# Performance work log

Hardware: AMD Instinct MI355X
Metric: run time of the kernel (lower is better)

The kernel has to match this reference:

```python
import math
import jax, jax.numpy as jnp
import numpy as np

E = 8          # num_experts
H = 1024       # hidden_dim
F = 2048       # ffn_dim
TOP_K = 2
CAP_FACTOR = 1.25
B, S = 2, 2048


def setup_inputs() -> dict:
    key = jax.random.key(0)
    ks = jax.random.split(key, 7)
    xavier_gu = math.sqrt(2.0 / (H + F))
    return {
        "x": jax.random.normal(ks[0], (B, S, H), dtype=jnp.float32),
        "router_weight": 0.01 * jax.random.normal(ks[1], (H, E), dtype=jnp.float32),
        "w_gate": xavier_gu * jax.random.normal(ks[2], (E, H, F), dtype=jnp.float32),
        "w_up": xavier_gu * jax.random.normal(ks[3], (E, H, F), dtype=jnp.float32),
        "w_down": xavier_gu * jax.random.normal(ks[4], (E, F, H), dtype=jnp.float32),
        "ln_gamma": jnp.ones((H,), dtype=jnp.float32),
        "ln_beta": jnp.zeros((H,), dtype=jnp.float32),
    }


def _layernorm(x, g, b, eps=1e-5):
    mu = x.mean(-1, keepdims=True)
    var = ((x - mu) ** 2).mean(-1, keepdims=True)
    return (x - mu) / jnp.sqrt(var + eps) * g + b


def reference(x, router_weight, w_gate, w_up, w_down, ln_gamma, ln_beta):
    Bd, Sd, Hd = x.shape
    T = Bd * Sd
    cap = int(math.ceil(CAP_FACTOR * T / E))  # static capacity per expert

    residual = x
    tokens = _layernorm(x, ln_gamma, ln_beta).reshape(T, Hd)

    # ---- router: softmax + top-k + renormalize ----
    logits = tokens @ router_weight                      # (T, E) fp32
    probs = jax.nn.softmax(logits, axis=-1)
    wts, idx = jax.lax.top_k(probs, TOP_K)               # (T, K)
    wts = wts / wts.sum(-1, keepdims=True)

    # ---- dispatch: first-come-first-served up to capacity per expert ----
    mask_all = (idx[None, :, :] == jnp.arange(E)[:, None, None]).any(-1)  # (E, T)
    # stable argsort puts routed token indices (in order) first
    sel = jnp.argsort(jnp.where(mask_all, 0, 1), axis=1, stable=True)[:, :cap]  # (E, cap)
    valid = jnp.take_along_axis(mask_all, sel, axis=1)   # (E, cap)
    xin = tokens[sel] * valid[..., None]                 # (E, cap, H); zeros for empty slots

    # ---- grouped SwiGLU expert GEMMs ----
    gate = jax.nn.silu(jnp.einsum('ech,ehf->ecf', xin, w_gate))
    up = jnp.einsum('ech,ehf->ecf', xin, w_up)
    expert_outputs = jnp.einsum('ecf,efh->ech', gate * up, w_down)  # (E, cap, H)

    # ---- scatter-gather combine (slot = min(t, cap-1), per reference impl) ----
    slot = jnp.minimum(jnp.arange(T), cap - 1)           # (T,)
    gathered = expert_outputs[idx, slot[:, None]]        # (T, K, H)
    out = (wts[..., None] * gathered).sum(axis=1)        # (T, H)

    return out.reshape(Bd, Sd, Hd) + residual
```

## Files before the change

### kernel.cpp

```cpp
#include <hip/hip_runtime.h>
#include <hip/hip_bf16.h>

#define NE 8
#define NH 1024
#define NF 2048
#define NT 4096
#define CAP 640

typedef __bf16 bf16x8 __attribute__((ext_vector_type(8)));
typedef float f32x4 __attribute__((ext_vector_type(4)));

__device__ __forceinline__ ushort f2bf(float f) {
    union { float f; unsigned u; } v; v.f = f;
    unsigned r = (v.u + 0x7FFFu + ((v.u >> 16) & 1u)) >> 16;
    return (ushort)r;
}

__device__ __forceinline__ void glds16(const ushort* g, ushort* l) {
    __builtin_amdgcn_global_load_lds((const __attribute__((address_space(1))) void*)g,
                                     (__attribute__((address_space(3))) void*)l,
                                     16, 0, 0);
}

__global__ __launch_bounds__(256) void k_transpose(
    const float* __restrict__ in, ushort* __restrict__ out, int R, int C)
{
    int e = blockIdx.z;
    int c0 = blockIdx.x * 64, r0 = blockIdx.y * 64;
    in  += (size_t)e * R * C;
    out += (size_t)e * R * C;

    __shared__ __align__(16) ushort lds[64 * 72];
    int t = threadIdx.x;
    int rl = t >> 4;
    int cl = (t & 15) * 4;

    #pragma unroll
    for (int i = 0; i < 4; ++i) {
        int r = i * 16 + rl;
        float4 v = *(const float4*)(in + (size_t)(r0 + r) * C + c0 + cl);
        lds[(cl + 0) * 72 + r] = f2bf(v.x);
        lds[(cl + 1) * 72 + r] = f2bf(v.y);
        lds[(cl + 2) * 72 + r] = f2bf(v.z);
        lds[(cl + 3) * 72 + r] = f2bf(v.w);
    }
    __syncthreads();

    int c = t >> 2, rq = (t & 3) * 16;
    uint4 a = *(const uint4*)&lds[c * 72 + rq];
    uint4 b = *(const uint4*)&lds[c * 72 + rq + 8];
    *(uint4*)(out + (size_t)(c0 + c) * R + r0 + rq)     = a;
    *(uint4*)(out + (size_t)(c0 + c) * R + r0 + rq + 8) = b;
}

__global__ __launch_bounds__(256) void k_ln_router(
    const float* __restrict__ x, const float* __restrict__ rw,
    const float* __restrict__ gamma, const float* __restrict__ beta,
    ushort* __restrict__ tok_bf, int* __restrict__ idx, float* __restrict__ wts)
{
    int t = blockIdx.x, tid = threadIdx.x;
    int lane = tid & 63, wid = tid >> 6;
    const float* xp = x + (size_t)t * NH;

    float4 v = *(const float4*)(xp + tid * 4);
    float xs[4] = {v.x, v.y, v.z, v.w};
    float s = xs[0] + xs[1] + xs[2] + xs[3];
    float q = xs[0]*xs[0] + xs[1]*xs[1] + xs[2]*xs[2] + xs[3]*xs[3];

    __shared__ float rs[4], rq[4], rl[4][8];
    #pragma unroll
    for (int o = 32; o; o >>= 1) { s += __shfl_xor(s, o); q += __shfl_xor(q, o); }
    if (lane == 0) { rs[wid] = s; rq[wid] = q; }
    __syncthreads();
    float S = rs[0] + rs[1] + rs[2] + rs[3];
    float Q = rq[0] + rq[1] + rq[2] + rq[3];
    float mean = S * (1.0f / NH);
    float var  = Q * (1.0f / NH) - mean * mean;
    float rstd = 1.0f / sqrtf(var + 1e-5f);

    float le[8] = {0,0,0,0,0,0,0,0};
    ushort tb[4];
    #pragma unroll
    for (int j = 0; j < 4; ++j) {
        int h = tid * 4 + j;
        float nh = (xs[j] - mean) * rstd * gamma[h] + beta[h];
        tb[j] = f2bf(nh);
        float4 r0 = *(const float4*)(rw + h * 8);
        float4 r1 = *(const float4*)(rw + h * 8 + 4);
        le[0] += nh * r0.x; le[1] += nh * r0.y; le[2] += nh * r0.z; le[3] += nh * r0.w;
        le[4] += nh * r1.x; le[5] += nh * r1.y; le[6] += nh * r1.z; le[7] += nh * r1.w;
    }
    union { ushort s2[4]; uint2 u2; } pk;
    pk.s2[0]=tb[0]; pk.s2[1]=tb[1]; pk.s2[2]=tb[2]; pk.s2[3]=tb[3];
    *(uint2*)(tok_bf + (size_t)t * NH + tid * 4) = pk.u2;

    #pragma unroll
    for (int o = 32; o; o >>= 1)
        #pragma unroll
        for (int e = 0; e < 8; ++e) le[e] += __shfl_xor(le[e], o);
    if (lane == 0)
        #pragma unroll
        for (int e = 0; e < 8; ++e) rl[wid][e] = le[e];
    __syncthreads();

    if (tid == 0) {
        float l[8];
        #pragma unroll
        for (int e = 0; e < 8; ++e) l[e] = rl[0][e] + rl[1][e] + rl[2][e] + rl[3][e];
        float mx = l[0];
        #pragma unroll
        for (int e = 1; e < 8; ++e) mx = fmaxf(mx, l[e]);
        float p[8], den = 0.f;
        #pragma unroll
        for (int e = 0; e < 8; ++e) { p[e] = expf(l[e] - mx); den += p[e]; }
        float rden = 1.0f / den;
        #pragma unroll
        for (int e = 0; e < 8; ++e) p[e] *= rden;
        int i0 = 0; float b0 = p[0];
        #pragma unroll
        for (int e = 1; e < 8; ++e) if (p[e] > b0) { b0 = p[e]; i0 = e; }
        int i1 = (i0 == 0) ? 1 : 0; float b1 = p[i1];
        #pragma unroll
        for (int e = 0; e < 8; ++e) if (e != i0 && p[e] > b1) { b1 = p[e]; i1 = e; }
        float sw = 1.0f / (b0 + b1);
        idx[2*t] = i0; idx[2*t+1] = i1;
        wts[2*t] = b0 * sw; wts[2*t+1] = b1 * sw;
    }
}

__global__ __launch_bounds__(1024) void k_build_sel(
    const int* __restrict__ idx, int* __restrict__ sel)
{
    int e = blockIdx.x, tid = threadIdx.x;
    int lane = tid & 63, wid = tid >> 6;
    __shared__ int wsum[16], wpre[16], sbase;
    if (tid < CAP) sel[e * CAP + tid] = -1;
    if (tid == 0) sbase = 0;
    __syncthreads();

    for (int ch = 0; ch < NT / 1024; ++ch) {
        int t = ch * 1024 + tid;
        int m = (idx[2*t] == e || idx[2*t+1] == e) ? 1 : 0;
        int v = m;
        #pragma unroll
        for (int d = 1; d < 64; d <<= 1) {
            int u = __shfl_up(v, d);
            if (lane >= d) v += u;
        }
        if (lane == 63) wsum[wid] = v;
        __syncthreads();
        if (tid < 16) {
            int ws = wsum[tid], wv = ws;
            #pragma unroll
            for (int d = 1; d < 16; d <<= 1) {
                int u = __shfl_up(wv, d);
                if (tid >= d) wv += u;
            }
            wpre[tid] = wv - ws;
        }
        __syncthreads();
        int base0 = sbase;
        int slot = base0 + wpre[wid] + v - m;
        if (m && slot < CAP) sel[e * CAP + slot] = t;
        __syncthreads();
        if (tid == 0) sbase = base0 + wpre[15] + wsum[15];
        __syncthreads();
    }
}

__global__ __launch_bounds__(256) void k_gather(
    const int* __restrict__ sel, const ushort* __restrict__ tok,
    ushort* __restrict__ xin)
{
    int sIdx = blockIdx.x;
    int tokid = sel[sIdx];
    uint2 v = make_uint2(0u, 0u);
    if (tokid >= 0)
        v = *(const uint2*)(tok + (size_t)tokid * NH + threadIdx.x * 4);
    *(uint2*)(xin + (size_t)sIdx * NH + threadIdx.x * 4) = v;
}

__global__ __launch_bounds__(256) void k_gemm1(
    const ushort* __restrict__ xin, const ushort* __restrict__ wgT,
    const ushort* __restrict__ wuT, ushort* __restrict__ hb)
{
    int e = blockIdx.z, mb = blockIdx.y, nb = blockIdx.x;
    const ushort* A  = xin + (size_t)e * CAP * NH + (size_t)mb * 128 * NH;
    const ushort* Bg = wgT + (size_t)e * NF * NH + (size_t)nb * 128 * NH;
    const ushort* Bu = wuT + (size_t)e * NF * NH + (size_t)nb * 128 * NH;
    ushort* out = hb + (size_t)e * CAP * NF + (size_t)mb * 128 * NF + nb * 128;

    __shared__ __align__(16) ushort Al[128 * 32];
    __shared__ __align__(16) ushort Bgl[128 * 32];
    __shared__ __align__(16) ushort Bul[128 * 32];

    int tid = threadIdx.x, lane = tid & 63, wid = tid >> 6;
    int wm = wid >> 1, wn = wid & 1;
    int lr = lane & 15, lq = lane >> 4;
    int ldrow = lane >> 2;
    int lcol  = (lane & 3) * 8;

    f32x4 accg[4][4] = {}; f32x4 accu[4][4] = {};

    for (int k0 = 0; k0 < NH; k0 += 32) {
        #pragma unroll
        for (int i = 0; i < 2; ++i) {
            int row = i * 64 + wid * 16 + ldrow;
            int lb  = i * 2048 + wid * 512;
            glds16(A  + (size_t)row * NH + k0 + lcol, Al  + lb);
            glds16(Bg + (size_t)row * NH + k0 + lcol, Bgl + lb);
            glds16(Bu + (size_t)row * NH + k0 + lcol, Bul + lb);
        }
        __syncthreads();

        bf16x8 af[4], bgf[4], buf_[4];
        #pragma unroll
        for (int m = 0; m < 4; ++m)
            af[m] = *(const bf16x8*)&Al[(wm * 64 + m * 16 + lr) * 32 + lq * 8];
        #pragma unroll
        for (int n = 0; n < 4; ++n) {
            bgf[n]  = *(const bf16x8*)&Bgl[(wn * 64 + n * 16 + lr) * 32 + lq * 8];
            buf_[n] = *(const bf16x8*)&Bul[(wn * 64 + n * 16 + lr) * 32 + lq * 8];
        }
        #pragma unroll
        for (int m = 0; m < 4; ++m)
            #pragma unroll
            for (int n = 0; n < 4; ++n) {
                accg[m][n] = __builtin_amdgcn_mfma_f32_16x16x32_bf16(af[m], bgf[n],  accg[m][n], 0, 0, 0);
                accu[m][n] = __builtin_amdgcn_mfma_f32_16x16x32_bf16(af[m], buf_[n], accu[m][n], 0, 0, 0);
            }
        __syncthreads();
    }

    #pragma unroll
    for (int m = 0; m < 4; ++m)
        #pragma unroll
        for (int n = 0; n < 4; ++n)
            #pragma unroll
            for (int r = 0; r < 4; ++r) {
                int row = wm * 64 + m * 16 + lq * 4 + r;
                int col = wn * 64 + n * 16 + lr;
                float g = accg[m][n][r], u = accu[m][n][r];
                float sg = g / (1.0f + expf(-g));
                out[(size_t)row * NF + col] = f2bf(sg * u);
            }
}

__global__ __launch_bounds__(256) void k_gemm2(
    const ushort* __restrict__ hb, const ushort* __restrict__ wdT,
    float* __restrict__ eo)
{
    int e = blockIdx.z, mb = blockIdx.y, nb = blockIdx.x;
    const ushort* A = hb  + (size_t)e * CAP * NF + (size_t)mb * 128 * NF;
    const ushort* B = wdT + (size_t)e * NH * NF + (size_t)nb * 64 * NF;
    float* out = eo + (size_t)e * CAP * NH + (size_t)mb * 128 * NH + nb * 64;

    __shared__ __align__(16) ushort Al[128 * 32];
    __shared__ __align__(16) ushort Bl[64 * 32];

    int tid = threadIdx.x, lane = tid & 63, wid = tid >> 6;
    int wm = wid >> 1, wn = wid & 1;
    int lr = lane & 15, lq = lane >> 4;
    int ldrow = lane >> 2;
    int lcol  = (lane & 3) * 8;

    f32x4 acc[4][2] = {};

    for (int k0 = 0; k0 < NF; k0 += 32) {
        #pragma unroll
        for (int i = 0; i < 2; ++i) {
            int row = i * 64 + wid * 16 + ldrow;
            glds16(A + (size_t)row * NF + k0 + lcol, Al + i * 2048 + wid * 512);
        }
        glds16(B + (size_t)(wid * 16 + ldrow) * NF + k0 + lcol, Bl + wid * 512);
        __syncthreads();

        bf16x8 af[4], bf_[2];
        #pragma unroll
        for (int m = 0; m < 4; ++m)
            af[m] = *(const bf16x8*)&Al[(wm * 64 + m * 16 + lr) * 32 + lq * 8];
        #pragma unroll
        for (int n = 0; n < 2; ++n)
            bf_[n] = *(const bf16x8*)&Bl[(wn * 32 + n * 16 + lr) * 32 + lq * 8];
        #pragma unroll
        for (int m = 0; m < 4; ++m)
            #pragma unroll
            for (int n = 0; n < 2; ++n)
                acc[m][n] = __builtin_amdgcn_mfma_f32_16x16x32_bf16(af[m], bf_[n], acc[m][n], 0, 0, 0);
        __syncthreads();
    }

    #pragma unroll
    for (int m = 0; m < 4; ++m)
        #pragma unroll
        for (int n = 0; n < 2; ++n)
            #pragma unroll
            for (int r = 0; r < 4; ++r) {
                int row = wm * 64 + m * 16 + lq * 4 + r;
                int col = wn * 32 + n * 16 + lr;
                out[(size_t)row * NH + col] = acc[m][n][r];
            }
}

__global__ __launch_bounds__(256) void k_final(
    const float* __restrict__ x, const float* __restrict__ eo,
    const int* __restrict__ idx, const float* __restrict__ wts,
    float* __restrict__ out)
{
    int t = blockIdx.x;
    int c = (t < CAP - 1) ? t : (CAP - 1);
    int e0 = idx[2*t], e1 = idx[2*t+1];
    float w0 = wts[2*t], w1 = wts[2*t+1];
    int h = threadIdx.x * 4;
    float4 xv = *(const float4*)(x + (size_t)t * NH + h);
    float4 a = *(const float4*)(eo + ((size_t)e0 * CAP + c) * NH + h);
    float4 b = *(const float4*)(eo + ((size_t)e1 * CAP + c) * NH + h);
    float4 o;
    o.x = xv.x + w0 * a.x + w1 * b.x;
    o.y = xv.y + w0 * a.y + w1 * b.y;
    o.z = xv.z + w0 * a.z + w1 * b.z;
    o.w = xv.w + w0 * a.w + w1 * b.w;
    *(float4*)(out + (size_t)t * NH + h) = o;
}

extern "C" void kernel_launch(void* const* d_in, const int* in_sizes, int n_in,
                              void* d_out, int out_size, void* d_ws, size_t ws_size,
                              hipStream_t stream)
{
    const float* x     = (const float*)d_in[0];
    const float* rw    = (const float*)d_in[1];
    const float* wg    = (const float*)d_in[2];
    const float* wu    = (const float*)d_in[3];
    const float* wd    = (const float*)d_in[4];
    const float* gamma = (const float*)d_in[5];
    const float* beta  = (const float*)d_in[6];
    float* out = (float*)d_out;

    char* ws = (char*)d_ws;
    ushort* tok_bf = (ushort*)(ws);
    ushort* xin    = (ushort*)(ws +   8388608);
    ushort* hb     = (ushort*)(ws +  18874368);
    float*  eo     = (float*) (ws +  39845888);
    ushort* wgT    = (ushort*)(ws +  60817408);
    ushort* wuT    = (ushort*)(ws +  94371840);
    ushort* wdT    = (ushort*)(ws + 127926272);
    int*    idx    = (int*)   (ws + 161480704);
    float*  wts    = (float*) (ws + 161513472);
    int*    sel    = (int*)   (ws + 161546240);

    k_transpose<<<dim3(NF / 64, NH / 64, NE), 256, 0, stream>>>(wg, wgT, NH, NF);
    k_transpose<<<dim3(NF / 64, NH / 64, NE), 256, 0, stream>>>(wu, wuT, NH, NF);
    k_transpose<<<dim3(NH / 64, NF / 64, NE), 256, 0, stream>>>(wd, wdT, NF, NH);

    k_ln_router<<<NT, 256, 0, stream>>>(x, rw, gamma, beta, tok_bf, idx, wts);
    k_build_sel<<<NE, 1024, 0, stream>>>(idx, sel);
    k_gather<<<NE * CAP, 256, 0, stream>>>(sel, tok_bf, xin);
    k_gemm1<<<dim3(NF / 128, CAP / 128, NE), 256, 0, stream>>>(xin, wgT, wuT, hb);
    k_gemm2<<<dim3(NH / 64, CAP / 128, NE), 256, 0, stream>>>(hb, wdT, eo);
    k_final<<<NT, 256, 0, stream>>>(x, eo, idx, wts, out);
}
```

Baseline: 421.3 us.

## Rewrite expert GEMMs with multi-stage async pipeline, swizzled LDS, larger tiles

Both expert GEMMs now use 512-thread blocks with 256-row tiles, a 4-slot LDS ring prefetched two steps ahead via direct global-to-LDS loads, XOR-swizzled LDS layouts, and manual waitcnt/barrier plus setprio around the MFMA bursts. Capacity is padded to 768 so the larger M tiles divide evenly, which adds wasted compute on the padded rows. The weight transpose-convert kernel is also replaced by a register-only column-strided version without LDS, and the workspace layout is reshuffled. The aim is to hide global load latency behind MFMA work and cut LDS bank conflicts and barrier stalls.

```diff
diff --git a/kernel.cpp b/kernel.cpp
--- a/kernel.cpp
+++ b/kernel.cpp
@@ -4,8 +4,9 @@
 #define NE 8
 #define NH 1024
 #define NF 2048
-#define NT 4096
+#define NT_TOK 4096
 #define CAP 640
+#define CAPP 768
 
 typedef __bf16 bf16x8 __attribute__((ext_vector_type(8)));
 typedef float f32x4 __attribute__((ext_vector_type(4)));
@@ -22,35 +23,26 @@
                                      16, 0, 0);
 }
 
-__global__ __launch_bounds__(256) void k_transpose(
+#define MFMA_BF16 __builtin_amdgcn_mfma_f32_16x16x32_bf16
+
+__global__ __launch_bounds__(256) void k_conv_t(
     const float* __restrict__ in, ushort* __restrict__ out, int R, int C)
 {
     int e = blockIdx.z;
-    int c0 = blockIdx.x * 64, r0 = blockIdx.y * 64;
+    int c  = blockIdx.x * 64 + (threadIdx.x & 63);
+    int rb = blockIdx.y * 128 + (threadIdx.x >> 6) * 32;
     in  += (size_t)e * R * C;
     out += (size_t)e * R * C;
-
-    __shared__ __align__(16) ushort lds[64 * 72];
-    int t = threadIdx.x;
-    int rl = t >> 4;
-    int cl = (t & 15) * 4;
-
-    #pragma unroll
-    for (int i = 0; i < 4; ++i) {
-        int r = i * 16 + rl;
-        float4 v = *(const float4*)(in + (size_t)(r0 + r) * C + c0 + cl);
-        lds[(cl + 0) * 72 + r] = f2bf(v.x);
-        lds[(cl + 1) * 72 + r] = f2bf(v.y);
-        lds[(cl + 2) * 72 + r] = f2bf(v.z);
-        lds[(cl + 3) * 72 + r] = f2bf(v.w);
-    }
-    __syncthreads();
-
-    int c = t >> 2, rq = (t & 3) * 16;
-    uint4 a = *(const uint4*)&lds[c * 72 + rq];
-    uint4 b = *(const uint4*)&lds[c * 72 + rq + 8];
-    *(uint4*)(out + (size_t)(c0 + c) * R + r0 + rq)     = a;
-    *(uint4*)(out + (size_t)(c0 + c) * R + r0 + rq + 8) = b;
+    float v[32];
+    #pragma unroll
+    for (int j = 0; j < 32; ++j) v[j] = in[(size_t)(rb + j) * C + c];
+    #pragma unroll
+    for (int q = 0; q < 4; ++q) {
+        union { ushort sh[8]; uint4 u; } p;
+        #pragma unroll
+        for (int j = 0; j < 8; ++j) p.sh[j] = f2bf(v[q * 8 + j]);
+        *(uint4*)(out + (size_t)c * R + rb + q * 8) = p.u;
+    }
 }
 
 __global__ __launch_bounds__(256) void k_ln_router(
@@ -134,11 +126,11 @@
     int e = blockIdx.x, tid = threadIdx.x;
     int lane = tid & 63, wid = tid >> 6;
     __shared__ int wsum[16], wpre[16], sbase;
-    if (tid < CAP) sel[e * CAP + tid] = -1;
+    if (tid < CAPP) sel[e * CAPP + tid] = -1;
     if (tid == 0) sbase = 0;
     __syncthreads();
 
-    for (int ch = 0; ch < NT / 1024; ++ch) {
+    for (int ch = 0; ch < NT_TOK / 1024; ++ch) {
         int t = ch * 1024 + tid;
         int m = (idx[2*t] == e || idx[2*t+1] == e) ? 1 : 0;
         int v = m;
@@ -161,7 +153,7 @@
         __syncthreads();
         int base0 = sbase;
         int slot = base0 + wpre[wid] + v - m;
-        if (m && slot < CAP) sel[e * CAP + slot] = t;
+        if (m && slot < CAP) sel[e * CAPP + slot] = t;
         __syncthreads();
         if (tid == 0) sbase = base0 + wpre[15] + wsum[15];
         __syncthreads();
@@ -180,58 +172,190 @@
     *(uint2*)(xin + (size_t)sIdx * NH + threadIdx.x * 4) = v;
 }
 
-__global__ __launch_bounds__(256) void k_gemm1(
+
+__global__ __launch_bounds__(512, 2) void k_gemm1(
     const ushort* __restrict__ xin, const ushort* __restrict__ wgT,
     const ushort* __restrict__ wuT, ushort* __restrict__ hb)
 {
+    __shared__ __align__(16) ushort As[4][8192];
+    __shared__ __align__(16) ushort Bgs[4][4096];
+    __shared__ __align__(16) ushort Bus[4][4096];
+
     int e = blockIdx.z, mb = blockIdx.y, nb = blockIdx.x;
-    const ushort* A  = xin + (size_t)e * CAP * NH + (size_t)mb * 128 * NH;
+    const ushort* A  = xin + (size_t)e * CAPP * NH + (size_t)mb * 256 * NH;
     const ushort* Bg = wgT + (size_t)e * NF * NH + (size_t)nb * 128 * NH;
     const ushort* Bu = wuT + (size_t)e * NF * NH + (size_t)nb * 128 * NH;
-    ushort* out = hb + (size_t)e * CAP * NF + (size_t)mb * 128 * NF + nb * 128;
-
-    __shared__ __align__(16) ushort Al[128 * 32];
-    __shared__ __align__(16) ushort Bgl[128 * 32];
-    __shared__ __align__(16) ushort Bul[128 * 32];
+
+    int tid = threadIdx.x, lane = tid & 63, wid = tid >> 6;
+    int wm = wid >> 2, wn = wid & 3;
+    int lr = lane & 15, lq = lane >> 4;
+
+    int Rg = tid >> 3;
+    int ug = (tid & 7) ^ (Rg & 7);
+    int sROW2 = ug >> 2;
+    int sCOL  = (ug & 3) * 8;
+    size_t aoffg0 = (size_t)(2 * Rg + sROW2) * NH + sCOL;
+    size_t aoffg1 = (size_t)(2 * (64 + Rg) + sROW2) * NH + sCOL;
+    size_t boffg  = (size_t)(2 * Rg + sROW2) * NH + sCOL;
+    int aldsu0 = (wid * 8) * 64;
+    int aldsu1 = (64 + wid * 8) * 64;
+    int bldsu  = wid * 512;
+
+    int aoff[8], goff[2];
+    #pragma unroll
+    for (int m = 0; m < 8; ++m) {
+        int a = wm * 128 + m * 16 + lr;
+        int Rr = a >> 1;
+        int sl = (((a & 1) << 2) | lq) ^ (Rr & 7);
+        aoff[m] = Rr * 64 + sl * 8;
+    }
+    #pragma unroll
+    for (int n = 0; n < 2; ++n) {
+        int nn = wn * 32 + n * 16 + lr;
+        int Rr = nn >> 1;
+        int sl = (((nn & 1) << 2) | lq) ^ (Rr & 7);
+        goff[n] = Rr * 64 + sl * 8;
+    }
+
+    f32x4 accg[8][2] = {}; f32x4 accu[8][2] = {};
+
+    const int NT = NH / 32;
+
+    #define STAGE1(t) do { int _sl = (t) & 3; int _k0 = (t) * 32;               \
+        glds16(A  + aoffg0 + _k0, &As[_sl][aldsu0]);                            \
+        glds16(A  + aoffg1 + _k0, &As[_sl][aldsu1]);                            \
+        glds16(Bg + boffg  + _k0, &Bgs[_sl][bldsu]);                            \
+        glds16(Bu + boffg  + _k0, &Bus[_sl][bldsu]); } while (0)
+
+    STAGE1(0); STAGE1(1);
+    asm volatile("s_waitcnt vmcnt(4)" ::: "memory");
+    asm volatile("s_barrier" ::: "memory");
+
+    for (int t = 0; t < NT; ++t) {
+        int slot = t & 3;
+        bool pf = (t + 2 < NT);
+        if (pf) STAGE1(t + 2);
+        const ushort* Ab = &As[slot][0];
+        const ushort* Gb = &Bgs[slot][0];
+        const ushort* Ub = &Bus[slot][0];
+        bf16x8 af[8], bg[2], bu[2];
+        #pragma unroll
+        for (int m = 0; m < 8; ++m) af[m] = *(const bf16x8*)&Ab[aoff[m]];
+        #pragma unroll
+        for (int n = 0; n < 2; ++n) {
+            bg[n] = *(const bf16x8*)&Gb[goff[n]];
+            bu[n] = *(const bf16x8*)&Ub[goff[n]];
+        }
+        __builtin_amdgcn_s_setprio(1);
+        #pragma unroll
+        for (int m = 0; m < 8; ++m)
+            #pragma unroll
+            for (int n = 0; n < 2; ++n) {
+                accg[m][n] = MFMA_BF16(af[m], bg[n], accg[m][n], 0, 0, 0);
+                accu[m][n] = MFMA_BF16(af[m], bu[n], accu[m][n], 0, 0, 0);
+            }
+        __builtin_amdgcn_s_setprio(0);
+        if (pf) asm volatile("s_waitcnt vmcnt(4)" ::: "memory");
+        else    asm volatile("s_waitcnt vmcnt(0)" ::: "memory");
+        asm volatile("s_barrier" ::: "memory");
+    }
+    #undef STAGE1
+
+    ushort* outp = hb + (size_t)e * CAPP * NF + (size_t)mb * 256 * NF + nb * 128;
+    #pragma unroll
+    for (int m = 0; m < 8; ++m)
+        #pragma unroll
+        for (int n = 0; n < 2; ++n)
+            #pragma unroll
+            for (int r = 0; r < 4; ++r) {
+                int row = wm * 128 + m * 16 + lq * 4 + r;
+                int col = wn * 32 + n * 16 + lr;
+                float g = accg[m][n][r], u = accu[m][n][r];
+                float sg = g / (1.0f + expf(-g));
+                outp[(size_t)row * NF + col] = f2bf(sg * u);
+            }
+}
+
+__global__ __launch_bounds__(512, 2) void k_gemm2(
+    const ushort* __restrict__ hb, const ushort* __restrict__ wdT,
+    float* __restrict__ eo)
+{
+    __shared__ __align__(16) ushort As[4][8192];
+    __shared__ __align__(16) ushort Bs[4][4096];
+
+    int e = blockIdx.z, mb = blockIdx.y, nb = blockIdx.x;
+    const ushort* A = hb  + (size_t)e * CAPP * NF + (size_t)mb * 256 * NF;
+    const ushort* B = wdT + (size_t)e * NH * NF + (size_t)nb * 128 * NF;
 
     int tid = threadIdx.x, lane = tid & 63, wid = tid >> 6;
     int wm = wid >> 1, wn = wid & 1;
     int lr = lane & 15, lq = lane >> 4;
-    int ldrow = lane >> 2;
-    int lcol  = (lane & 3) * 8;
-
-    f32x4 accg[4][4] = {}; f32x4 accu[4][4] = {};
-
-    for (int k0 = 0; k0 < NH; k0 += 32) {
-        #pragma unroll
-        for (int i = 0; i < 2; ++i) {
-            int row = i * 64 + wid * 16 + ldrow;
-            int lb  = i * 2048 + wid * 512;
-            glds16(A  + (size_t)row * NH + k0 + lcol, Al  + lb);
-            glds16(Bg + (size_t)row * NH + k0 + lcol, Bgl + lb);
-            glds16(Bu + (size_t)row * NH + k0 + lcol, Bul + lb);
-        }
-        __syncthreads();
-
-        bf16x8 af[4], bgf[4], buf_[4];
-        #pragma unroll
-        for (int m = 0; m < 4; ++m)
-            af[m] = *(const bf16x8*)&Al[(wm * 64 + m * 16 + lr) * 32 + lq * 8];
-        #pragma unroll
-        for (int n = 0; n < 4; ++n) {
-            bgf[n]  = *(const bf16x8*)&Bgl[(wn * 64 + n * 16 + lr) * 32 + lq * 8];
-            buf_[n] = *(const bf16x8*)&Bul[(wn * 64 + n * 16 + lr) * 32 + lq * 8];
-        }
+
+    int Rg = tid >> 3;
+    int ug = (tid & 7) ^ (Rg & 7);
+    int sROW2 = ug >> 2;
+    int sCOL  = (ug & 3) * 8;
+    size_t aoffg0 = (size_t)(2 * Rg + sROW2) * NF + sCOL;
+    size_t aoffg1 = (size_t)(2 * (64 + Rg) + sROW2) * NF + sCOL;
+    size_t boffg  = (size_t)(2 * Rg + sROW2) * NF + sCOL;
+    int aldsu0 = (wid * 8) * 64;
+    int aldsu1 = (64 + wid * 8) * 64;
+    int bldsu  = wid * 512;
+
+    int aoff[4], boff[4];
+    #pragma unroll
+    for (int m = 0; m < 4; ++m) {
+        int a = wm * 64 + m * 16 + lr;
+        int Rr = a >> 1;
+        int sl = (((a & 1) << 2) | lq) ^ (Rr & 7);
+        aoff[m] = Rr * 64 + sl * 8;
+    }
+    #pragma unroll
+    for (int n = 0; n < 4; ++n) {
+        int nn = wn * 64 + n * 16 + lr;
+        int Rr = nn >> 1;
+        int sl = (((nn & 1) << 2) | lq) ^ (Rr & 7);
+        boff[n] = Rr * 64 + sl * 8;
+    }
+
+    f32x4 acc[4][4] = {};
+
+    const int NT = NF / 32;
+
+    #define STAGE2(t) do { int _sl = (t) & 3; int _k0 = (t) * 32;               \
+        glds16(A + aoffg0 + _k0, &As[_sl][aldsu0]);                             \
+        glds16(A + aoffg1 + _k0, &As[_sl][aldsu1]);                             \
+        glds16(B + boffg  + _k0, &Bs[_sl][bldsu]); } while (0)
+
+    STAGE2(0); STAGE2(1);
+    asm volatile("s_waitcnt vmcnt(3)" ::: "memory");
+    asm volatile("s_barrier" ::: "memory");
+
+    for (int t = 0; t < NT; ++t) {
+        int slot = t & 3;
+        bool pf = (t + 2 < NT);
+        if (pf) STAGE2(t + 2);
+        const ushort* Ab = &As[slot][0];
+        const ushort* Bb = &Bs[slot][0];
+        bf16x8 af[4], bf_[4];
+        #pragma unroll
+        for (int m = 0; m < 4; ++m) af[m] = *(const bf16x8*)&Ab[aoff[m]];
+        #pragma unroll
+        for (int n = 0; n < 4; ++n) bf_[n] = *(const bf16x8*)&Bb[boff[n]];
+        __builtin_amdgcn_s_setprio(1);
         #pragma unroll
         for (int m = 0; m < 4; ++m)
             #pragma unroll
-            for (int n = 0; n < 4; ++n) {
-                accg[m][n] = __builtin_amdgcn_mfma_f32_16x16x32_bf16(af[m], bgf[n],  accg[m][n], 0, 0, 0);
-                accu[m][n] = __builtin_amdgcn_mfma_f32_16x16x32_bf16(af[m], buf_[n], accu[m][n], 0, 0, 0);
-            }
-        __syncthreads();
-    }
-
+            for (int n = 0; n < 4; ++n)
+                acc[m][n] = MFMA_BF16(af[m], bf_[n], acc[m][n], 0, 0, 0);
+        __builtin_amdgcn_s_setprio(0);
+        if (pf) asm volatile("s_waitcnt vmcnt(3)" ::: "memory");
+        else    asm volatile("s_waitcnt vmcnt(0)" ::: "memory");
+        asm volatile("s_barrier" ::: "memory");
+    }
+    #undef STAGE2
+
+    float* outp = eo + (size_t)e * CAPP * NH + (size_t)mb * 256 * NH + nb * 128;
     #pragma unroll
     for (int m = 0; m < 4; ++m)
         #pragma unroll
@@ -240,65 +364,7 @@
             for (int r = 0; r < 4; ++r) {
                 int row = wm * 64 + m * 16 + lq * 4 + r;
                 int col = wn * 64 + n * 16 + lr;
-                float g = accg[m][n][r], u = accu[m][n][r];
-                float sg = g / (1.0f + expf(-g));
-                out[(size_t)row * NF + col] = f2bf(sg * u);
-            }
-}
-
-__global__ __launch_bounds__(256) void k_gemm2(
-    const ushort* __restrict__ hb, const ushort* __restrict__ wdT,
-    float* __restrict__ eo)
-{
-    int e = blockIdx.z, mb = blockIdx.y, nb = blockIdx.x;
-    const ushort* A = hb  + (size_t)e * CAP * NF + (size_t)mb * 128 * NF;
-    const ushort* B = wdT + (size_t)e * NH * NF + (size_t)nb * 64 * NF;
-    float* out = eo + (size_t)e * CAP * NH + (size_t)mb * 128 * NH + nb * 64;
-
-    __shared__ __align__(16) ushort Al[128 * 32];
-    __shared__ __align__(16) ushort Bl[64 * 32];
-
-    int tid = threadIdx.x, lane = tid & 63, wid = tid >> 6;
-    int wm = wid >> 1, wn = wid & 1;
-    int lr = lane & 15, lq = lane >> 4;
-    int ldrow = lane >> 2;
-    int lcol  = (lane & 3) * 8;
-
-    f32x4 acc[4][2] = {};
-
-    for (int k0 = 0; k0 < NF; k0 += 32) {
-        #pragma unroll
-        for (int i = 0; i < 2; ++i) {
-            int row = i * 64 + wid * 16 + ldrow;
-            glds16(A + (size_t)row * NF + k0 + lcol, Al + i * 2048 + wid * 512);
-        }
-        glds16(B + (size_t)(wid * 16 + ldrow) * NF + k0 + lcol, Bl + wid * 512);
-        __syncthreads();
-
-        bf16x8 af[4], bf_[2];
-        #pragma unroll
-        for (int m = 0; m < 4; ++m)
-            af[m] = *(const bf16x8*)&Al[(wm * 64 + m * 16 + lr) * 32 + lq * 8];
-        #pragma unroll
-        for (int n = 0; n < 2; ++n)
-            bf_[n] = *(const bf16x8*)&Bl[(wn * 32 + n * 16 + lr) * 32 + lq * 8];
-        #pragma unroll
-        for (int m = 0; m < 4; ++m)
-            #pragma unroll
-            for (int n = 0; n < 2; ++n)
-                acc[m][n] = __builtin_amdgcn_mfma_f32_16x16x32_bf16(af[m], bf_[n], acc[m][n], 0, 0, 0);
-        __syncthreads();
-    }
-
-    #pragma unroll
-    for (int m = 0; m < 4; ++m)
-        #pragma unroll
-        for (int n = 0; n < 2; ++n)
-            #pragma unroll
-            for (int r = 0; r < 4; ++r) {
-                int row = wm * 64 + m * 16 + lq * 4 + r;
-                int col = wn * 32 + n * 16 + lr;
-                out[(size_t)row * NH + col] = acc[m][n][r];
+                outp[(size_t)row * NH + col] = acc[m][n][r];
             }
 }
 
@@ -313,8 +379,8 @@
     float w0 = wts[2*t], w1 = wts[2*t+1];
     int h = threadIdx.x * 4;
     float4 xv = *(const float4*)(x + (size_t)t * NH + h);
-    float4 a = *(const float4*)(eo + ((size_t)e0 * CAP + c) * NH + h);
-    float4 b = *(const float4*)(eo + ((size_t)e1 * CAP + c) * NH + h);
+    float4 a = *(const float4*)(eo + ((size_t)e0 * CAPP + c) * NH + h);
+    float4 b = *(const float4*)(eo + ((size_t)e1 * CAPP + c) * NH + h);
     float4 o;
     o.x = xv.x + w0 * a.x + w1 * b.x;
     o.y = xv.y + w0 * a.y + w1 * b.y;
@@ -337,25 +403,25 @@
     float* out = (float*)d_out;
 
     char* ws = (char*)d_ws;
+    float*  eo     = (float*) (ws);
     ushort* tok_bf = (ushort*)(ws);
-    ushort* xin    = (ushort*)(ws +   8388608);
-    ushort* hb     = (ushort*)(ws +  18874368);
-    float*  eo     = (float*) (ws +  39845888);
-    ushort* wgT    = (ushort*)(ws +  60817408);
-    ushort* wuT    = (ushort*)(ws +  94371840);
-    ushort* wdT    = (ushort*)(ws + 127926272);
-    int*    idx    = (int*)   (ws + 161480704);
-    float*  wts    = (float*) (ws + 161513472);
-    int*    sel    = (int*)   (ws + 161546240);
-
-    k_transpose<<<dim3(NF / 64, NH / 64, NE), 256, 0, stream>>>(wg, wgT, NH, NF);
-    k_transpose<<<dim3(NF / 64, NH / 64, NE), 256, 0, stream>>>(wu, wuT, NH, NF);
-    k_transpose<<<dim3(NH / 64, NF / 64, NE), 256, 0, stream>>>(wd, wdT, NF, NH);
-
-    k_ln_router<<<NT, 256, 0, stream>>>(x, rw, gamma, beta, tok_bf, idx, wts);
+    ushort* xin    = (ushort*)(ws +  25165824);
+    ushort* hb     = (ushort*)(ws +  37748736);
+    ushort* wgT    = (ushort*)(ws +  62914560);
+    ushort* wuT    = (ushort*)(ws +  96468992);
+    ushort* wdT    = (ushort*)(ws + 130023424);
+    int*    idx    = (int*)   (ws + 163577856);
+    float*  wts    = (float*) (ws + 163610624);
+    int*    sel    = (int*)   (ws + 163643392);
+
+    k_conv_t<<<dim3(NF / 64, NH / 128, NE), 256, 0, stream>>>(wg, wgT, NH, NF);
+    k_conv_t<<<dim3(NF / 64, NH / 128, NE), 256, 0, stream>>>(wu, wuT, NH, NF);
+    k_conv_t<<<dim3(NH / 64, NF / 128, NE), 256, 0, stream>>>(wd, wdT, NF, NH);
+
+    k_ln_router<<<NT_TOK, 256, 0, stream>>>(x, rw, gamma, beta, tok_bf, idx, wts);
     k_build_sel<<<NE, 1024, 0, stream>>>(idx, sel);
-    k_gather<<<NE * CAP, 256, 0, stream>>>(sel, tok_bf, xin);
-    k_gemm1<<<dim3(NF / 128, CAP / 128, NE), 256, 0, stream>>>(xin, wgT, wuT, hb);
-    k_gemm2<<<dim3(NH / 64, CAP / 128, NE), 256, 0, stream>>>(hb, wdT, eo);
-    k_final<<<NT, 256, 0, stream>>>(x, eo, idx, wts, out);
-}
+    k_gather<<<NE * CAPP, 256, 0, stream>>>(sel, tok_bf, xin);
+    k_gemm1<<<dim3(NF / 128, CAPP / 256, NE), 512, 0, stream>>>(xin, wgT, wuT, hb);
+    k_gemm2<<<dim3(NH / 128, CAPP / 256, NE), 512, 0, stream>>>(hb, wdT, eo);
+    k_final<<<NT_TOK, 256, 0, stream>>>(x, eo, idx, wts, out);
+}
```

Measured after the change: 443.1 us. 5.2% more time.
